# Performance work log

Measured on AMD Instinct MI355X. Metric: run time of the kernel, lower is better.

Reference implementation:

```python
import jax, jax.numpy as jnp
import numpy as np

N = 50000        # nodes
E = 800000       # edges (avg degree 16)
IN = 128         # n_feat
C0, H0 = 32, 4   # layer0: out_channels, heads (concat -> 128)
C1, H1 = 32, 1   # layer1: out_channels, heads (mean)
NEG_SLOPE = 0.2


def setup_inputs() -> dict:
    key = jax.random.key(0)
    ks = jax.random.split(key, 16)
    def p(k, shape, fan):
        return jax.random.normal(k, shape, jnp.float32) / np.float32(np.sqrt(fan))
    x = jax.random.normal(ks[0], (N, IN), jnp.float32)
    edge_index = jax.random.randint(ks[1], (2, E), 0, N, dtype=jnp.int32)
    return {
        "x": x,
        "edge_index": edge_index,
        # layer 0 GATConv: in=128 -> 4 heads x 32, concat
        "W0": p(ks[2], (H0 * C0, IN), IN),
        "att_src0": p(ks[3], (H0, C0), C0),
        "att_dst0": p(ks[4], (H0, C0), C0),
        "bias0": jnp.zeros((H0 * C0,), jnp.float32),
        "linW0": p(ks[5], (H0 * C0, IN), IN),
        "linb0": jnp.zeros((H0 * C0,), jnp.float32),
        # layer 1 GATConv: in=128 -> 1 head x 32, mean
        "W1": p(ks[6], (H1 * C1, H0 * C0), H0 * C0),
        "att_src1": p(ks[7], (H1, C1), C1),
        "att_dst1": p(ks[8], (H1, C1), C1),
        "bias1": jnp.zeros((C1,), jnp.float32),
        "linW1": p(ks[9], (C1, H0 * C0), H0 * C0),
        "linb1": jnp.zeros((C1,), jnp.float32),
    }


def gat_conv(x, src, dst, W, att_src, att_dst, bias, concat):
    """PyG-style GATConv (self-loops already appended to src/dst)."""
    n = x.shape[0]
    H, C = att_src.shape
    h = (x @ W.T).reshape(n, H, C)                       # [N,H,C]
    a_src = jnp.einsum('nhc,hc->nh', h, att_src)          # [N,H]
    a_dst = jnp.einsum('nhc,hc->nh', h, att_dst)          # [N,H]
    e = jax.nn.leaky_relu(a_src[src] + a_dst[dst], NEG_SLOPE)  # [E,H]
    # segment softmax over incoming edges of each dst node
    m = jax.ops.segment_max(e, dst, num_segments=n)       # [N,H]
    ex = jnp.exp(e - m[dst])
    denom = jax.ops.segment_sum(ex, dst, num_segments=n)  # [N,H]
    alpha = ex / (denom[dst] + 1e-16)                     # [E,H]
    out = jax.ops.segment_sum(h[src] * alpha[:, :, None], dst, num_segments=n)  # [N,H,C]
    out = out.reshape(n, H * C) if concat else out.mean(axis=1)
    return out + bias


def reference(x, edge_index, W0, att_src0, att_dst0, bias0, linW0, linb0,
              W1, att_src1, att_dst1, bias1, linW1, linb1):
    n = x.shape[0]
    loop = jnp.arange(n, dtype=edge_index.dtype)
    src = jnp.concatenate([edge_index[0], loop])  # add self-loops
    dst = jnp.concatenate([edge_index[1], loop])
    # layer 0: conv + linear skip, then ELU (eval mode -> dropout is a no-op)
    h = gat_conv(x, src, dst, W0, att_src0, att_dst0, bias0, True) + x @ linW0.T + linb0
    h = jax.nn.elu(h)
    # layer 1 (last): conv + linear skip, no activation
    out = gat_conv(h, src, dst, W1, att_src1, att_dst1, bias1, False) + h @ linW1.T + linb1
    return out
```

## Files before the change

### kernel.cpp

```cpp
#include <hip/hip_runtime.h>
#include <hip/hip_bf16.h>


typedef __attribute__((ext_vector_type(8))) short bf8_t;
typedef __attribute__((ext_vector_type(4))) float f4_t;
typedef __attribute__((ext_vector_type(2))) float f2_t;

#define NBUCK 256
#define BCAP  8192

__device__ inline short f2bf(float f) {
    return (short)__builtin_bit_cast(unsigned short, __float2bfloat16(f));
}
__device__ inline float blo(unsigned int p) { return __uint_as_float(p << 16); }
__device__ inline float bhi(unsigned int p) { return __uint_as_float(p & 0xffff0000u); }
__device__ inline float lrexp(float e) {
    e = (e > 0.f) ? e : 0.2f * e;
    return __expf(e);
}

__global__ void k_gz(int* __restrict__ gcur) {
    gcur[threadIdx.x] = threadIdx.x * BCAP;
}

__global__ __launch_bounds__(256) void k_initbucket(
    const int* __restrict__ ei,
    const float* __restrict__ W0, const float* __restrict__ lW0,
    const float* __restrict__ W1, const float* __restrict__ lW1,
    const float* __restrict__ b0, const float* __restrict__ lb0,
    const float* __restrict__ b1, const float* __restrict__ lb1,
    short* __restrict__ Wp0, short* __restrict__ lWp0,
    short* __restrict__ Wp1, short* __restrict__ lWp1,
    float* __restrict__ bc0, float* __restrict__ bc1,
    int* __restrict__ gcur,
    unsigned int* __restrict__ bucketed, int E, int T) {
    __shared__ int hist[NBUCK];
    __shared__ int gbase[NBUCK];
    int tid = threadIdx.x;

    if (blockIdx.x < 64) {
        int i = blockIdx.x * 256 + tid;
        {
            int j = i & 7, lane = (i >> 3) & 63, kc = i >> 9;
            int kb = kc & 3, ct = kc >> 2;
            int src = (ct * 16 + (lane & 15)) * 128 + kb * 32 + (lane >> 4) * 8 + j;
            Wp0[i]  = f2bf(W0[src]);
            lWp0[i] = f2bf(lW0[src]);
            if (i < 4096) {
                Wp1[i]  = f2bf(W1[src]);
                lWp1[i] = f2bf(lW1[src]);
            }
        }
        if (i < 128) bc0[i] = b0[i] + lb0[i];
        else if (i < 160) bc1[i - 128] = b1[i - 128] + lb1[i - 128];
        return;
    }

    int bb = blockIdx.x - 64;
    hist[tid] = 0;
    __syncthreads();
    int base = bb * 2048;
    unsigned int pk[8]; int rk[8]; int bk[8];
    #pragma unroll
    for (int j = 0; j < 8; j++) {
        int e = base + j * 256 + tid;
        if (e < T) {
            int src, dst;
            if (e < E) { src = ei[e]; dst = ei[E + e]; }
            else       { src = e - E; dst = src; }
            int b = dst >> 8;
            pk[j] = ((unsigned int)dst << 16) | (unsigned int)src;
            bk[j] = b;
            rk[j] = atomicAdd(&hist[b], 1);
        } else bk[j] = -1;
    }
    __syncthreads();
    int h = hist[tid];
    if (h > 0) gbase[tid] = atomicAdd(&gcur[tid], h);
    __syncthreads();
    #pragma unroll
    for (int j = 0; j < 8; j++)
        if (bk[j] >= 0)
            bucketed[gbase[bk[j]] + rk[j]] = pk[j];
}


#define TSTR 136

__global__ __launch_bounds__(256) void k_fillgemm0(
    const unsigned int* __restrict__ bucketed, const int* __restrict__ gcur,
    int* __restrict__ rowstart,
    unsigned short* __restrict__ esrc,
    const float* __restrict__ x,
    const short* __restrict__ Wp0, const short* __restrict__ lWp0,
    const float* __restrict__ as0, const float* __restrict__ ad0,
    unsigned char* __restrict__ h0f8, __hip_bfloat16* __restrict__ skipb,
    float* __restrict__ a0s, float* __restrict__ a0d, int N) {
    __shared__ int ihist[256];
    __shared__ int incl[256];
    __shared__ short tile[4][16 * TSTR];
    __shared__ unsigned char t8[4][16 * 136];
    int NBK = (N + 255) >> 8;

    if ((int)blockIdx.x < NBK) {
        int b = blockIdx.x, t = threadIdx.x;
        int nodebase = b << 8;
        int cntt = gcur[t] - t * BCAP;
        incl[t] = cntt;
        __syncthreads();
        for (int off = 1; off < 256; off <<= 1) {
            int tv = (t >= off) ? incl[t - off] : 0;
            __syncthreads();
            incl[t] += tv;
            __syncthreads();
        }
        int rbase = (b > 0) ? incl[b - 1] : 0;
        if (b == 0 && t == 255) rowstart[N] = incl[255];
        int used = gcur[b] - b * BCAP;
        const unsigned int* bk = bucketed + (size_t)b * BCAP;
        __syncthreads();
        ihist[t] = 0;
        __syncthreads();
        for (int i = t; i < used; i += 256)
            atomicAdd(&ihist[(bk[i] >> 16) - nodebase], 1);
        __syncthreads();
        int v = ihist[t];
        incl[t] = v;
        __syncthreads();
        for (int off = 1; off < 256; off <<= 1) {
            int tv = (t >= off) ? incl[t - off] : 0;
            __syncthreads();
            incl[t] += tv;
            __syncthreads();
        }
        int myexcl = incl[t] - v;
        int node = nodebase + t;
        if (node < N) rowstart[node] = rbase + myexcl;
        __syncthreads();
        ihist[t] = myexcl;
        __syncthreads();
        for (int i = t; i < used; i += 256) {
            unsigned int p = bk[i];
            int pos = atomicAdd(&ihist[(p >> 16) - nodebase], 1);
            esrc[rbase + pos] = (unsigned short)(p & 0xffffu);
        }
        return;
    }

    int bx = blockIdx.x - NBK;
    int wv = threadIdx.x >> 6, lane = threadIdx.x & 63;
    int rowbase = bx * 64 + wv * 16;
    int m = lane & 15, q = lane >> 4;
    int arow = rowbase + m; if (arow >= N) arow = N - 1;
    bf8_t a[4];
    #pragma unroll
    for (int kb = 0; kb < 4; kb++) {
        const float4* px = (const float4*)(x + (size_t)arow * 128 + kb * 32 + q * 8);
        float4 lo = px[0], hi = px[1];
        bf8_t f;
        f[0] = f2bf(lo.x); f[1] = f2bf(lo.y); f[2] = f2bf(lo.z); f[3] = f2bf(lo.w);
        f[4] = f2bf(hi.x); f[5] = f2bf(hi.y); f[6] = f2bf(hi.z); f[7] = f2bf(hi.w);
        a[kb] = f;
    }
    float sacc[4][4], dacc[4][4];
    #pragma unroll
    for (int h = 0; h < 4; h++)
        #pragma unroll
        for (int r = 0; r < 4; r++) { sacc[h][r] = 0.f; dacc[h][r] = 0.f; }
    short* tl = tile[wv];
    unsigned char* t8l = t8[wv];
    int r4 = lane >> 2, qt = lane & 3;
    int drow = rowbase + r4;

    #pragma unroll
    for (int ct = 0; ct < 8; ct++) {
        f4_t acc = {0.f, 0.f, 0.f, 0.f};
        #pragma unroll
        for (int kb = 0; kb < 4; kb++) {
            bf8_t b = *(const bf8_t*)(Wp0 + (((ct * 4 + kb) * 64 + lane) << 3));
            acc = __builtin_amdgcn_mfma_f32_16x16x32_bf16(a[kb], b, acc, 0, 0, 0);
        }
        int hd = ct >> 1;
        float ws = as0[ct * 16 + m], wd = ad0[ct * 16 + m];
        #pragma unroll
        for (int r = 0; r < 4; r++) {
            sacc[hd][r] += acc[r] * ws;
            dacc[hd][r] += acc[r] * wd;
            int pk8 = __builtin_amdgcn_cvt_pk_fp8_f32(acc[r], acc[r], 0, false);
            t8l[(q * 4 + r) * 136 + ct * 16 + m] = (unsigned char)(pk8 & 0xff);
        }
    }
    if (drow < N) {
        const unsigned char* sp8 = t8l + r4 * 136 + qt * 32;
        uint2 w0 = ((const uint2*)sp8)[0];
        uint2 w1 = ((const uint2*)sp8)[1];
        uint2 w2 = ((const uint2*)sp8)[2];
        uint2 w3 = ((const uint2*)sp8)[3];
        uint4 o0 = make_uint4(w0.x, w0.y, w1.x, w1.y);
        uint4 o1 = make_uint4(w2.x, w2.y, w3.x, w3.y);
        unsigned char* dst = h0f8 + (size_t)drow * 128 + qt * 32;
        *(uint4*)dst = o0;
        *(uint4*)(dst + 16) = o1;
    }

    #pragma unroll
    for (int ct = 0; ct < 8; ct++) {
        f4_t acc = {0.f, 0.f, 0.f, 0.f};
        #pragma unroll
        for (int kb = 0; kb < 4; kb++) {
            bf8_t b = *(const bf8_t*)(lWp0 + (((ct * 4 + kb) * 64 + lane) << 3));
            acc = __builtin_amdgcn_mfma_f32_16x16x32_bf16(a[kb], b, acc, 0, 0, 0);
        }
        #pragma unroll
        for (int r = 0; r < 4; r++)
            tl[(q * 4 + r) * TSTR + ct * 16 + m] = f2bf(acc[r]);
    }
    if (drow < N) {
        short* dst = (short*)skipb + (size_t)drow * 128 + qt * 32;
        const short* srcp = tl + r4 * TSTR + qt * 32;
        #pragma unroll
        for (int s = 0; s < 4; s++)
            *(uint4*)(dst + s * 8) = *(const uint4*)(srcp + s * 8);
    }

    #pragma unroll
    for (int h = 0; h < 4; h++)
        #pragma unroll
        for (int r = 0; r < 4; r++) {
            float s = sacc[h][r], d = dacc[h][r];
            #pragma unroll
            for (int off = 1; off < 16; off <<= 1) {
                s += __shfl_xor(s, off);
                d += __shfl_xor(d, off);
            }
            sacc[h][r] = s; dacc[h][r] = d;
        }
    if (m < 4) {
        #pragma unroll
        for (int r = 0; r < 4; r++) {
            int row = rowbase + q * 4 + r;
            if (row < N) {
                float sv = (m == 0) ? sacc[0][r] : (m == 1) ? sacc[1][r]
                         : (m == 2) ? sacc[2][r] : sacc[3][r];
                float dv = (m == 0) ? dacc[0][r] : (m == 1) ? dacc[1][r]
                         : (m == 2) ? dacc[2][r] : dacc[3][r];
                a0s[row * 4 + m] = sv;
                a0d[row * 4 + m] = dv;
            }
        }
    }
}


__global__ __launch_bounds__(256) void k_gemm1(
    const __hip_bfloat16* __restrict__ hin,
    const short* __restrict__ Wp1, const short* __restrict__ lWp1,
    const float* __restrict__ as1, const float* __restrict__ ad1,
    __hip_bfloat16* __restrict__ h1, float* __restrict__ skipb ,
    float* __restrict__ a1s, float* __restrict__ a1d, int N) {
    __shared__ short th[4][16 * 40];
    __shared__ float ts[4][16 * 36];
    int wv = threadIdx.x >> 6, lane = threadIdx.x & 63;
    int rowbase = blockIdx.x * 64 + wv * 16;
    int m = lane & 15, q = lane >> 4;
    int arow = rowbase + m; if (arow >= N) arow = N - 1;
    const short* xs = (const short*)hin;
    bf8_t a[4];
    #pragma unroll
    for (int kb = 0; kb < 4; kb++)
        a[kb] = *(const bf8_t*)(xs + (size_t)arow * 128 + kb * 32 + q * 8);
    float sacc[4], dacc[4];
    #pragma unroll
    for (int r = 0; r < 4; r++) { sacc[r] = 0.f; dacc[r] = 0.f; }
    short* tlh = th[wv];
    float* tls = ts[wv];
    int r4 = lane >> 2, qt = lane & 3;
    int drow = rowbase + r4;

    #pragma unroll
    for (int ct = 0; ct < 2; ct++) {
        f4_t acc = {0.f, 0.f, 0.f, 0.f};
        #pragma unroll
        for (int kb = 0; kb < 4; kb++) {
            bf8_t b = *(const bf8_t*)(Wp1 + (((ct * 4 + kb) * 64 + lane) << 3));
            acc = __builtin_amdgcn_mfma_f32_16x16x32_bf16(a[kb], b, acc, 0, 0, 0);
        }
        float ws = as1[ct * 16 + m], wd = ad1[ct * 16 + m];
        #pragma unroll
        for (int r = 0; r < 4; r++) {
            sacc[r] += acc[r] * ws;
            dacc[r] += acc[r] * wd;
            tlh[(q * 4 + r) * 40 + ct * 16 + m] = f2bf(acc[r]);
        }
    }
    #pragma unroll
    for (int ct = 0; ct < 2; ct++) {
        f4_t acc = {0.f, 0.f, 0.f, 0.f};
        #pragma unroll
        for (int kb = 0; kb < 4; kb++) {
            bf8_t b = *(const bf8_t*)(lWp1 + (((ct * 4 + kb) * 64 + lane) << 3));
            acc = __builtin_amdgcn_mfma_f32_16x16x32_bf16(a[kb], b, acc, 0, 0, 0);
        }
        #pragma unroll
        for (int r = 0; r < 4; r++)
            tls[(q * 4 + r) * 36 + ct * 16 + m] = acc[r];
    }
    if (drow < N) {
        *(uint4*)((short*)h1 + (size_t)drow * 32 + qt * 8) =
            *(const uint4*)(tlh + r4 * 40 + qt * 8);
        float* dst = skipb + (size_t)drow * 32 + qt * 8;
        const float* srcp = tls + r4 * 36 + qt * 8;
        *(uint4*)(dst) = *(const uint4*)(srcp);
        *(uint4*)(dst + 4) = *(const uint4*)(srcp + 4);
    }
    #pragma unroll
    for (int r = 0; r < 4; r++) {
        float s = sacc[r], d = dacc[r];
        #pragma unroll
        for (int off = 1; off < 16; off <<= 1) {
            s += __shfl_xor(s, off);
            d += __shfl_xor(d, off);
        }
        if (m == 0) {
            int row = rowbase + q * 4 + r;
            if (row < N) { a1s[row] = s; a1d[row] = d; }
        }
    }
}


__global__ __launch_bounds__(256) void k_agg0(
    const int* __restrict__ rowstart, const unsigned short* __restrict__ esrc,
    const uint2* __restrict__ h0f8,
    const float* __restrict__ a0s, const float* __restrict__ a0d,
    const float* __restrict__ bc0,
    unsigned int* __restrict__ h1in_u,
    int n) {
    int node = (blockIdx.x * 256 + threadIdx.x) >> 6;
    int lane = threadIdx.x & 63;
    if (node >= n) return;
    int g = lane >> 4, t = lane & 15, hd = t >> 2;
    float ad = a0d[node * 4 + hd];
    int s0 = rowstart[node], s1 = rowstart[node + 1];
    float den = 0.f;
    float acc[8];
    #pragma unroll
    for (int k = 0; k < 8; k++) acc[k] = 0.f;
    int i = s0 + g;
    for (; i + 12 < s1; i += 16) {
        int sE[4]; float e[4]; uint2 p[4];
        #pragma unroll
        for (int j = 0; j < 4; j++) sE[j] = esrc[i + 4 * j];
        #pragma unroll
        for (int j = 0; j < 4; j++) e[j] = a0s[sE[j] * 4 + hd] + ad;
        #pragma unroll
        for (int j = 0; j < 4; j++) p[j] = h0f8[(size_t)sE[j] * 16 + t];
        #pragma unroll
        for (int j = 0; j < 4; j++) {
            float wgt = lrexp(e[j]);
            den += wgt;
            f2_t c01 = __builtin_amdgcn_cvt_pk_f32_fp8(p[j].x, false);
            f2_t c23 = __builtin_amdgcn_cvt_pk_f32_fp8(p[j].x, true);
            f2_t c45 = __builtin_amdgcn_cvt_pk_f32_fp8(p[j].y, false);
            f2_t c67 = __builtin_amdgcn_cvt_pk_f32_fp8(p[j].y, true);
            acc[0] += wgt * c01.x; acc[1] += wgt * c01.y;
            acc[2] += wgt * c23.x; acc[3] += wgt * c23.y;
            acc[4] += wgt * c45.x; acc[5] += wgt * c45.y;
            acc[6] += wgt * c67.x; acc[7] += wgt * c67.y;
        }
    }
    for (; i < s1; i += 4) {
        int s = esrc[i];
        float wgt = lrexp(a0s[s * 4 + hd] + ad);
        uint2 p = h0f8[(size_t)s * 16 + t];
        den += wgt;
        f2_t c01 = __builtin_amdgcn_cvt_pk_f32_fp8(p.x, false);
        f2_t c23 = __builtin_amdgcn_cvt_pk_f32_fp8(p.x, true);
        f2_t c45 = __builtin_amdgcn_cvt_pk_f32_fp8(p.y, false);
        f2_t c67 = __builtin_amdgcn_cvt_pk_f32_fp8(p.y, true);
        acc[0] += wgt * c01.x; acc[1] += wgt * c01.y;
        acc[2] += wgt * c23.x; acc[3] += wgt * c23.y;
        acc[4] += wgt * c45.x; acc[5] += wgt * c45.y;
        acc[6] += wgt * c67.x; acc[7] += wgt * c67.y;
    }
    #pragma unroll
    for (int k = 0; k < 8; k++) {
        acc[k] += __shfl_xor(acc[k], 16);
        acc[k] += __shfl_xor(acc[k], 32);
    }
    den += __shfl_xor(den, 16);
    den += __shfl_xor(den, 32);
    if (g == 0) {
        float inv = 1.0f / (den + 1e-16f);
        uint4 sp = *(const uint4*)(h1in_u + (size_t)node * 64 + t * 4);
        int c0 = t * 8;
        float o[8];
        o[0] = acc[0] * inv + blo(sp.x) + bc0[c0 + 0];
        o[1] = acc[1] * inv + bhi(sp.x) + bc0[c0 + 1];
        o[2] = acc[2] * inv + blo(sp.y) + bc0[c0 + 2];
        o[3] = acc[3] * inv + bhi(sp.y) + bc0[c0 + 3];
        o[4] = acc[4] * inv + blo(sp.z) + bc0[c0 + 4];
        o[5] = acc[5] * inv + bhi(sp.z) + bc0[c0 + 5];
        o[6] = acc[6] * inv + blo(sp.w) + bc0[c0 + 6];
        o[7] = acc[7] * inv + bhi(sp.w) + bc0[c0 + 7];
        #pragma unroll
        for (int k = 0; k < 8; k++)
            o[k] = (o[k] > 0.f) ? o[k] : (__expf(o[k]) - 1.f);
        uint4 res;
        res.x = (unsigned int)(unsigned short)f2bf(o[0]) | ((unsigned int)(unsigned short)f2bf(o[1]) << 16);
        res.y = (unsigned int)(unsigned short)f2bf(o[2]) | ((unsigned int)(unsigned short)f2bf(o[3]) << 16);
        res.z = (unsigned int)(unsigned short)f2bf(o[4]) | ((unsigned int)(unsigned short)f2bf(o[5]) << 16);
        res.w = (unsigned int)(unsigned short)f2bf(o[6]) | ((unsigned int)(unsigned short)f2bf(o[7]) << 16);
        *(uint4*)(h1in_u + (size_t)node * 64 + t * 4) = res;
    }
}

__global__ __launch_bounds__(256) void k_agg1(
    const int* __restrict__ rowstart, const unsigned short* __restrict__ esrc,
    const __hip_bfloat16* __restrict__ h1,
    const float* __restrict__ a1s, const float* __restrict__ a1d,
    const float* __restrict__ bc1,
    float* __restrict__ out, int n) {
    int node = (blockIdx.x * 256 + threadIdx.x) >> 6;
    int lane = threadIdx.x & 63;
    if (node >= n) return;
    int g = lane >> 4, t = lane & 15;
    float ad = a1d[node];
    int s0 = rowstart[node], s1 = rowstart[node + 1];
    const unsigned int* h1w = (const unsigned int*)h1;
    float den = 0.f, acc0 = 0.f, acc1 = 0.f;
    int i = s0 + g;
    for (; i + 12 < s1; i += 16) {
        int sE[4]; float e[4]; unsigned int p[4];
        #pragma unroll
        for (int j = 0; j < 4; j++) sE[j] = esrc[i + 4 * j];
        #pragma unroll
        for (int j = 0; j < 4; j++) e[j] = a1s[sE[j]] + ad;
        #pragma unroll
        for (int j = 0; j < 4; j++) p[j] = h1w[(size_t)sE[j] * 16 + t];
        #pragma unroll
        for (int j = 0; j < 4; j++) {
            float wgt = lrexp(e[j]);
            den += wgt;
            acc0 += wgt * blo(p[j]);
            acc1 += wgt * bhi(p[j]);
        }
    }
    for (; i < s1; i += 4) {
        int s = esrc[i];
        float wv = lrexp(a1s[s] + ad);
        unsigned int p = h1w[(size_t)s * 16 + t];
        den += wv; acc0 += wv * blo(p); acc1 += wv * bhi(p);
    }
    acc0 += __shfl_xor(acc0, 16); acc0 += __shfl_xor(acc0, 32);
    acc1 += __shfl_xor(acc1, 16); acc1 += __shfl_xor(acc1, 32);
    den  += __shfl_xor(den, 16);  den  += __shfl_xor(den, 32);
    if (g == 0) {
        float inv = 1.0f / (den + 1e-16f);
        int c0 = t * 2;
        size_t idx = (size_t)node * 32 + c0;
        float2 sk = *(const float2*)(out + idx);
        float2 r;
        r.x = acc0 * inv + sk.x + bc1[c0];
        r.y = acc1 * inv + sk.y + bc1[c0 + 1];
        *(float2*)(out + idx) = r;
    }
}


extern "C" void kernel_launch(void* const* d_in, const int* in_sizes, int n_in,
                              void* d_out, int out_size, void* d_ws, size_t ws_size,
                              hipStream_t stream) {
    const float* x   = (const float*)d_in[0];
    const int*   ei  = (const int*)d_in[1];
    const float* W0  = (const float*)d_in[2];
    const float* as0 = (const float*)d_in[3];
    const float* ad0 = (const float*)d_in[4];
    const float* b0  = (const float*)d_in[5];
    const float* lW0 = (const float*)d_in[6];
    const float* lb0 = (const float*)d_in[7];
    const float* W1  = (const float*)d_in[8];
    const float* as1 = (const float*)d_in[9];
    const float* ad1 = (const float*)d_in[10];
    const float* b1  = (const float*)d_in[11];
    const float* lW1 = (const float*)d_in[12];
    const float* lb1 = (const float*)d_in[13];
    float* out = (float*)d_out;

    const int N = in_sizes[0] / 128;
    const int E = in_sizes[1] / 2;
    const int T = E + N;
    const int NBK  = (N + 255) >> 8;
    const int NBBK = (T + 2047) / 2048;

    char* w = (char*)d_ws;
    auto alloc = [&](size_t bytes) -> char* {
        char* p = w; w += (bytes + 255) / 256 * 256; return p;
    };
    int* rowstart  = (int*)alloc((size_t)(N + 1) * 4);
    int* gcur      = (int*)alloc(NBUCK * 4);
    unsigned int* bucketed = (unsigned int*)alloc((size_t)NBUCK * BCAP * 4);
    unsigned short* esrc = (unsigned short*)alloc((size_t)T * 2);
    float* aS      = (float*)alloc((size_t)N * 4 * 4);
    float* aD      = (float*)alloc((size_t)N * 4 * 4);
    char* hbuf     = alloc((size_t)N * 128 * 2);
    __hip_bfloat16* h1in = (__hip_bfloat16*)alloc((size_t)N * 128 * 2);
    short* Wp0  = (short*)alloc(16384 * 2);
    short* lWp0 = (short*)alloc(16384 * 2);
    short* Wp1  = (short*)alloc(4096 * 2);
    short* lWp1 = (short*)alloc(4096 * 2);
    float* bc0  = (float*)alloc(128 * 4);
    float* bc1  = (float*)alloc(32 * 4);

    k_gz<<<1, NBUCK, 0, stream>>>(gcur);
    k_initbucket<<<64 + NBBK, 256, 0, stream>>>(ei, W0, lW0, W1, lW1,
                                                b0, lb0, b1, lb1,
                                                Wp0, lWp0, Wp1, lWp1, bc0, bc1,
                                                gcur, bucketed, E, T);
    k_fillgemm0<<<NBK + (N + 63) / 64, 256, 0, stream>>>(
        bucketed, gcur, rowstart, esrc,
        x, Wp0, lWp0, as0, ad0, (unsigned char*)hbuf, h1in, aS, aD, N);
    k_agg0<<<(N + 3) / 4, 256, 0, stream>>>(rowstart, esrc, (const uint2*)hbuf,
                                            aS, aD, bc0, (unsigned int*)h1in, N);
    k_gemm1<<<(N + 63) / 64, 256, 0, stream>>>(h1in, Wp1, lWp1, as1, ad1,
                                               (__hip_bfloat16*)hbuf, out, aS, aD, N);
    k_agg1<<<(N + 3) / 4, 256, 0, stream>>>(rowstart, esrc, (const __hip_bfloat16*)hbuf,
                                            aS, aD, bc1, out, N);
}
```

Baseline: 200.4 us.

## Fuse layer-0 aggregation with layer-1 GEMM and replace counter init kernel with memset

The layer-0 attention aggregation and the layer-1 projection/skip GEMM now run in a single kernel. Each 256-thread block aggregates 16 nodes (16 threads per node) into shared memory, then runs MFMA on that tile, so the ELU output no longer goes through global memory. The bucket-counter init kernel becomes a hipMemsetAsync, with the bucket base offset moved into the atomic add. The cost is less per-node parallelism in aggregation (one 16-lane group walks all edges of a node sequentially) and an extra block barrier before the GEMM.

```diff
diff --git a/kernel.cpp b/kernel.cpp
--- a/kernel.cpp
+++ b/kernel.cpp
@@ -17,10 +17,6 @@
 __device__ inline float lrexp(float e) {
     e = (e > 0.f) ? e : 0.2f * e;
     return __expf(e);
-}
-
-__global__ void k_gz(int* __restrict__ gcur) {
-    gcur[threadIdx.x] = threadIdx.x * BCAP;
 }
 
 __global__ __launch_bounds__(256) void k_initbucket(
@@ -76,7 +72,7 @@
     }
     __syncthreads();
     int h = hist[tid];
-    if (h > 0) gbase[tid] = atomicAdd(&gcur[tid], h);
+    if (h > 0) gbase[tid] = tid * BCAP + atomicAdd(&gcur[tid], h);
     __syncthreads();
     #pragma unroll
     for (int j = 0; j < 8; j++)
@@ -105,7 +101,7 @@
     if ((int)blockIdx.x < NBK) {
         int b = blockIdx.x, t = threadIdx.x;
         int nodebase = b << 8;
-        int cntt = gcur[t] - t * BCAP;
+        int cntt = gcur[t];
         incl[t] = cntt;
         __syncthreads();
         for (int off = 1; off < 256; off <<= 1) {
@@ -116,7 +112,7 @@
         }
         int rbase = (b > 0) ? incl[b - 1] : 0;
         if (b == 0 && t == 255) rowstart[N] = incl[255];
-        int used = gcur[b] - b * BCAP;
+        int used = gcur[b];
         const unsigned int* bk = bucketed + (size_t)b * BCAP;
         __syncthreads();
         ihist[t] = 0;
@@ -252,147 +248,72 @@
 }
 
 
-__global__ __launch_bounds__(256) void k_gemm1(
-    const __hip_bfloat16* __restrict__ hin,
-    const short* __restrict__ Wp1, const short* __restrict__ lWp1,
-    const float* __restrict__ as1, const float* __restrict__ ad1,
-    __hip_bfloat16* __restrict__ h1, float* __restrict__ skipb ,
-    float* __restrict__ a1s, float* __restrict__ a1d, int N) {
-    __shared__ short th[4][16 * 40];
-    __shared__ float ts[4][16 * 36];
-    int wv = threadIdx.x >> 6, lane = threadIdx.x & 63;
-    int rowbase = blockIdx.x * 64 + wv * 16;
-    int m = lane & 15, q = lane >> 4;
-    int arow = rowbase + m; if (arow >= N) arow = N - 1;
-    const short* xs = (const short*)hin;
-    bf8_t a[4];
-    #pragma unroll
-    for (int kb = 0; kb < 4; kb++)
-        a[kb] = *(const bf8_t*)(xs + (size_t)arow * 128 + kb * 32 + q * 8);
-    float sacc[4], dacc[4];
-    #pragma unroll
-    for (int r = 0; r < 4; r++) { sacc[r] = 0.f; dacc[r] = 0.f; }
-    short* tlh = th[wv];
-    float* tls = ts[wv];
-    int r4 = lane >> 2, qt = lane & 3;
-    int drow = rowbase + r4;
-
-    #pragma unroll
-    for (int ct = 0; ct < 2; ct++) {
-        f4_t acc = {0.f, 0.f, 0.f, 0.f};
-        #pragma unroll
-        for (int kb = 0; kb < 4; kb++) {
-            bf8_t b = *(const bf8_t*)(Wp1 + (((ct * 4 + kb) * 64 + lane) << 3));
-            acc = __builtin_amdgcn_mfma_f32_16x16x32_bf16(a[kb], b, acc, 0, 0, 0);
-        }
-        float ws = as1[ct * 16 + m], wd = ad1[ct * 16 + m];
-        #pragma unroll
-        for (int r = 0; r < 4; r++) {
-            sacc[r] += acc[r] * ws;
-            dacc[r] += acc[r] * wd;
-            tlh[(q * 4 + r) * 40 + ct * 16 + m] = f2bf(acc[r]);
-        }
-    }
-    #pragma unroll
-    for (int ct = 0; ct < 2; ct++) {
-        f4_t acc = {0.f, 0.f, 0.f, 0.f};
-        #pragma unroll
-        for (int kb = 0; kb < 4; kb++) {
-            bf8_t b = *(const bf8_t*)(lWp1 + (((ct * 4 + kb) * 64 + lane) << 3));
-            acc = __builtin_amdgcn_mfma_f32_16x16x32_bf16(a[kb], b, acc, 0, 0, 0);
-        }
-        #pragma unroll
-        for (int r = 0; r < 4; r++)
-            tls[(q * 4 + r) * 36 + ct * 16 + m] = acc[r];
-    }
-    if (drow < N) {
-        *(uint4*)((short*)h1 + (size_t)drow * 32 + qt * 8) =
-            *(const uint4*)(tlh + r4 * 40 + qt * 8);
-        float* dst = skipb + (size_t)drow * 32 + qt * 8;
-        const float* srcp = tls + r4 * 36 + qt * 8;
-        *(uint4*)(dst) = *(const uint4*)(srcp);
-        *(uint4*)(dst + 4) = *(const uint4*)(srcp + 4);
-    }
-    #pragma unroll
-    for (int r = 0; r < 4; r++) {
-        float s = sacc[r], d = dacc[r];
-        #pragma unroll
-        for (int off = 1; off < 16; off <<= 1) {
-            s += __shfl_xor(s, off);
-            d += __shfl_xor(d, off);
-        }
-        if (m == 0) {
-            int row = rowbase + q * 4 + r;
-            if (row < N) { a1s[row] = s; a1d[row] = d; }
-        }
-    }
-}
-
-
-__global__ __launch_bounds__(256) void k_agg0(
+__global__ __launch_bounds__(256) void k_aggfuse(
     const int* __restrict__ rowstart, const unsigned short* __restrict__ esrc,
     const uint2* __restrict__ h0f8,
     const float* __restrict__ a0s, const float* __restrict__ a0d,
     const float* __restrict__ bc0,
-    unsigned int* __restrict__ h1in_u,
-    int n) {
-    int node = (blockIdx.x * 256 + threadIdx.x) >> 6;
-    int lane = threadIdx.x & 63;
-    if (node >= n) return;
-    int g = lane >> 4, t = lane & 15, hd = t >> 2;
-    float ad = a0d[node * 4 + hd];
-    int s0 = rowstart[node], s1 = rowstart[node + 1];
-    float den = 0.f;
-    float acc[8];
-    #pragma unroll
-    for (int k = 0; k < 8; k++) acc[k] = 0.f;
-    int i = s0 + g;
-    for (; i + 12 < s1; i += 16) {
-        int sE[4]; float e[4]; uint2 p[4];
-        #pragma unroll
-        for (int j = 0; j < 4; j++) sE[j] = esrc[i + 4 * j];
-        #pragma unroll
-        for (int j = 0; j < 4; j++) e[j] = a0s[sE[j] * 4 + hd] + ad;
-        #pragma unroll
-        for (int j = 0; j < 4; j++) p[j] = h0f8[(size_t)sE[j] * 16 + t];
-        #pragma unroll
-        for (int j = 0; j < 4; j++) {
-            float wgt = lrexp(e[j]);
+    const unsigned int* __restrict__ skip0,
+    const short* __restrict__ Wp1, const short* __restrict__ lWp1,
+    const float* __restrict__ as1, const float* __restrict__ ad1,
+    __hip_bfloat16* __restrict__ h1, float* __restrict__ outskip,
+    float* __restrict__ a1s, float* __restrict__ a1d, int n) {
+    __shared__ __align__(16) short hrow[16][136];
+    __shared__ __align__(16) short th[16 * 40];
+    __shared__ __align__(16) float ts[16 * 36];
+    __shared__ float satt[2][16], datt[2][16];
+
+    int tid = threadIdx.x;
+    int nl = tid >> 4, t = tid & 15, hd = t >> 2;
+    int rowbase = blockIdx.x << 4;
+    int node = rowbase + nl;
+
+    if (node < n) {
+        float ad = a0d[node * 4 + hd];
+        int s0 = rowstart[node], s1 = rowstart[node + 1];
+        float den = 0.f;
+        float acc[8];
+        #pragma unroll
+        for (int k = 0; k < 8; k++) acc[k] = 0.f;
+        int i = s0;
+        for (; i + 3 < s1; i += 4) {
+            int sE[4]; float e[4]; uint2 p[4];
+            #pragma unroll
+            for (int j = 0; j < 4; j++) sE[j] = esrc[i + j];
+            #pragma unroll
+            for (int j = 0; j < 4; j++) e[j] = a0s[sE[j] * 4 + hd] + ad;
+            #pragma unroll
+            for (int j = 0; j < 4; j++) p[j] = h0f8[(size_t)sE[j] * 16 + t];
+            #pragma unroll
+            for (int j = 0; j < 4; j++) {
+                float wgt = lrexp(e[j]);
+                den += wgt;
+                f2_t c01 = __builtin_amdgcn_cvt_pk_f32_fp8(p[j].x, false);
+                f2_t c23 = __builtin_amdgcn_cvt_pk_f32_fp8(p[j].x, true);
+                f2_t c45 = __builtin_amdgcn_cvt_pk_f32_fp8(p[j].y, false);
+                f2_t c67 = __builtin_amdgcn_cvt_pk_f32_fp8(p[j].y, true);
+                acc[0] += wgt * c01.x; acc[1] += wgt * c01.y;
+                acc[2] += wgt * c23.x; acc[3] += wgt * c23.y;
+                acc[4] += wgt * c45.x; acc[5] += wgt * c45.y;
+                acc[6] += wgt * c67.x; acc[7] += wgt * c67.y;
+            }
+        }
+        for (; i < s1; ++i) {
+            int s = esrc[i];
+            float wgt = lrexp(a0s[s * 4 + hd] + ad);
+            uint2 p = h0f8[(size_t)s * 16 + t];
             den += wgt;
-            f2_t c01 = __builtin_amdgcn_cvt_pk_f32_fp8(p[j].x, false);
-            f2_t c23 = __builtin_amdgcn_cvt_pk_f32_fp8(p[j].x, true);
-            f2_t c45 = __builtin_amdgcn_cvt_pk_f32_fp8(p[j].y, false);
-            f2_t c67 = __builtin_amdgcn_cvt_pk_f32_fp8(p[j].y, true);
+            f2_t c01 = __builtin_amdgcn_cvt_pk_f32_fp8(p.x, false);
+            f2_t c23 = __builtin_amdgcn_cvt_pk_f32_fp8(p.x, true);
+            f2_t c45 = __builtin_amdgcn_cvt_pk_f32_fp8(p.y, false);
+            f2_t c67 = __builtin_amdgcn_cvt_pk_f32_fp8(p.y, true);
             acc[0] += wgt * c01.x; acc[1] += wgt * c01.y;
             acc[2] += wgt * c23.x; acc[3] += wgt * c23.y;
             acc[4] += wgt * c45.x; acc[5] += wgt * c45.y;
             acc[6] += wgt * c67.x; acc[7] += wgt * c67.y;
         }
-    }
-    for (; i < s1; i += 4) {
-        int s = esrc[i];
-        float wgt = lrexp(a0s[s * 4 + hd] + ad);
-        uint2 p = h0f8[(size_t)s * 16 + t];
-        den += wgt;
-        f2_t c01 = __builtin_amdgcn_cvt_pk_f32_fp8(p.x, false);
-        f2_t c23 = __builtin_amdgcn_cvt_pk_f32_fp8(p.x, true);
-        f2_t c45 = __builtin_amdgcn_cvt_pk_f32_fp8(p.y, false);
-        f2_t c67 = __builtin_amdgcn_cvt_pk_f32_fp8(p.y, true);
-        acc[0] += wgt * c01.x; acc[1] += wgt * c01.y;
-        acc[2] += wgt * c23.x; acc[3] += wgt * c23.y;
-        acc[4] += wgt * c45.x; acc[5] += wgt * c45.y;
-        acc[6] += wgt * c67.x; acc[7] += wgt * c67.y;
-    }
-    #pragma unroll
-    for (int k = 0; k < 8; k++) {
-        acc[k] += __shfl_xor(acc[k], 16);
-        acc[k] += __shfl_xor(acc[k], 32);
-    }
-    den += __shfl_xor(den, 16);
-    den += __shfl_xor(den, 32);
-    if (g == 0) {
         float inv = 1.0f / (den + 1e-16f);
-        uint4 sp = *(const uint4*)(h1in_u + (size_t)node * 64 + t * 4);
+        uint4 sp = *(const uint4*)(skip0 + (size_t)node * 64 + t * 4);
         int c0 = t * 8;
         float o[8];
         o[0] = acc[0] * inv + blo(sp.x) + bc0[c0 + 0];
@@ -411,9 +332,65 @@
         res.y = (unsigned int)(unsigned short)f2bf(o[2]) | ((unsigned int)(unsigned short)f2bf(o[3]) << 16);
         res.z = (unsigned int)(unsigned short)f2bf(o[4]) | ((unsigned int)(unsigned short)f2bf(o[5]) << 16);
         res.w = (unsigned int)(unsigned short)f2bf(o[6]) | ((unsigned int)(unsigned short)f2bf(o[7]) << 16);
-        *(uint4*)(h1in_u + (size_t)node * 64 + t * 4) = res;
-    }
-}
+        *(uint4*)&hrow[nl][t * 8] = res;
+    } else {
+        *(uint4*)&hrow[nl][t * 8] = make_uint4(0u, 0u, 0u, 0u);
+    }
+    __syncthreads();
+
+    int wv = tid >> 6, lane = tid & 63;
+    int m = lane & 15, q = lane >> 4;
+    bf8_t a[4];
+    #pragma unroll
+    for (int kb = 0; kb < 4; kb++)
+        a[kb] = *(const bf8_t*)&hrow[m][kb * 32 + q * 8];
+    int ct = wv & 1;
+    const short* Wt = (wv < 2) ? Wp1 : lWp1;
+    f4_t acc = {0.f, 0.f, 0.f, 0.f};
+    #pragma unroll
+    for (int kb = 0; kb < 4; kb++) {
+        bf8_t b = *(const bf8_t*)(Wt + (((ct * 4 + kb) * 64 + lane) << 3));
+        acc = __builtin_amdgcn_mfma_f32_16x16x32_bf16(a[kb], b, acc, 0, 0, 0);
+    }
+    if (wv < 2) {
+        float wsv = as1[ct * 16 + m], wdv = ad1[ct * 16 + m];
+        #pragma unroll
+        for (int r = 0; r < 4; r++) {
+            th[(q * 4 + r) * 40 + ct * 16 + m] = f2bf(acc[r]);
+            float s = acc[r] * wsv, d = acc[r] * wdv;
+            #pragma unroll
+            for (int off = 1; off < 16; off <<= 1) {
+                s += __shfl_xor(s, off);
+                d += __shfl_xor(d, off);
+            }
+            if (m == 0) { satt[ct][q * 4 + r] = s; datt[ct][q * 4 + r] = d; }
+        }
+    } else {
+        #pragma unroll
+        for (int r = 0; r < 4; r++)
+            ts[(q * 4 + r) * 36 + ct * 16 + m] = acc[r];
+    }
+    __syncthreads();
+
+    if (tid < 64) {
+        int row = tid >> 2, qt = tid & 3;
+        if (rowbase + row < n)
+            *(uint4*)((short*)h1 + (size_t)(rowbase + row) * 32 + qt * 8) =
+                *(const uint4*)&th[row * 40 + qt * 8];
+    } else if (tid < 192) {
+        int i2 = tid - 64, row = i2 >> 3, qt = i2 & 7;
+        if (rowbase + row < n)
+            *(uint4*)(outskip + (size_t)(rowbase + row) * 32 + qt * 4) =
+                *(const uint4*)&ts[row * 36 + qt * 4];
+    } else if (tid < 208) {
+        int r2 = tid - 192;
+        if (rowbase + r2 < n) {
+            a1s[rowbase + r2] = satt[0][r2] + satt[1][r2];
+            a1d[rowbase + r2] = datt[0][r2] + datt[1][r2];
+        }
+    }
+}
+
 
 __global__ __launch_bounds__(256) void k_agg1(
     const int* __restrict__ rowstart, const unsigned short* __restrict__ esrc,
@@ -503,8 +480,11 @@
     unsigned short* esrc = (unsigned short*)alloc((size_t)T * 2);
     float* aS      = (float*)alloc((size_t)N * 4 * 4);
     float* aD      = (float*)alloc((size_t)N * 4 * 4);
-    char* hbuf     = alloc((size_t)N * 128 * 2);
-    __hip_bfloat16* h1in = (__hip_bfloat16*)alloc((size_t)N * 128 * 2);
+    char* hbuf     = alloc((size_t)N * 128);
+    __hip_bfloat16* skip0 = (__hip_bfloat16*)alloc((size_t)N * 128 * 2);
+    __hip_bfloat16* h1buf = (__hip_bfloat16*)alloc((size_t)N * 32 * 2);
+    float* aS1     = (float*)alloc((size_t)N * 4);
+    float* aD1     = (float*)alloc((size_t)N * 4);
     short* Wp0  = (short*)alloc(16384 * 2);
     short* lWp0 = (short*)alloc(16384 * 2);
     short* Wp1  = (short*)alloc(4096 * 2);
@@ -512,18 +492,18 @@
     float* bc0  = (float*)alloc(128 * 4);
     float* bc1  = (float*)alloc(32 * 4);
 
-    k_gz<<<1, NBUCK, 0, stream>>>(gcur);
+    hipMemsetAsync(gcur, 0, NBUCK * sizeof(int), stream);
     k_initbucket<<<64 + NBBK, 256, 0, stream>>>(ei, W0, lW0, W1, lW1,
                                                 b0, lb0, b1, lb1,
                                                 Wp0, lWp0, Wp1, lWp1, bc0, bc1,
                                                 gcur, bucketed, E, T);
     k_fillgemm0<<<NBK + (N + 63) / 64, 256, 0, stream>>>(
         bucketed, gcur, rowstart, esrc,
-        x, Wp0, lWp0, as0, ad0, (unsigned char*)hbuf, h1in, aS, aD, N);
-    k_agg0<<<(N + 3) / 4, 256, 0, stream>>>(rowstart, esrc, (const uint2*)hbuf,
-                                            aS, aD, bc0, (unsigned int*)h1in, N);
-    k_gemm1<<<(N + 63) / 64, 256, 0, stream>>>(h1in, Wp1, lWp1, as1, ad1,
-                                               (__hip_bfloat16*)hbuf, out, aS, aD, N);
-    k_agg1<<<(N + 3) / 4, 256, 0, stream>>>(rowstart, esrc, (const __hip_bfloat16*)hbuf,
-                                            aS, aD, bc1, out, N);
-}
+        x, Wp0, lWp0, as0, ad0, (unsigned char*)hbuf, skip0, aS, aD, N);
+    k_aggfuse<<<(N + 15) / 16, 256, 0, stream>>>(
+        rowstart, esrc, (const uint2*)hbuf, aS, aD, bc0,
+        (const unsigned int*)skip0, Wp1, lWp1, as1, ad1,
+        h1buf, out, aS1, aD1, N);
+    k_agg1<<<(N + 3) / 4, 256, 0, stream>>>(rowstart, esrc, h1buf,
+                                            aS1, aD1, bc1, out, N);
+}
```

Result: faster. 187.6 us (-6.4%).
